# Kernel optimization log

Hardware: AMD Instinct MI355X
Metric: run time of the kernel (lower is better)

## Reference

```python
import jax, jax.numpy as jnp
import numpy as np

H = 8        # n_heads (== n_kv_heads)
D = 128      # head_dim
WINDOW = 16  # sliding window (left); causal => right window = 0
EPS = 1e-6   # qk_norm_eps


def rms_norm(x, w, eps=EPS):
    # RMSNorm over last dim with learnable scale
    ms = jnp.mean(jnp.square(x), axis=-1, keepdims=True)
    return x * jax.lax.rsqrt(ms + eps) * w


def setup_inputs() -> dict:
    key = jax.random.key(0)
    ks = jax.random.split(key, 5)
    B, S, dim = 4, 2048, 1024
    scale = 1.0 / np.sqrt(dim)
    return {
        "x": jax.random.normal(ks[0], (B, S, dim), jnp.float32),
        "wq": jax.random.normal(ks[1], (dim, dim), jnp.float32) * scale,
        "wk": jax.random.normal(ks[2], (dim, dim), jnp.float32) * scale,
        "wv": jax.random.normal(ks[3], (dim, dim), jnp.float32) * scale,
        "wo": jax.random.normal(ks[4], (dim, dim), jnp.float32) * scale,
        "q_norm_w": jnp.ones((dim,), jnp.float32),
        "k_norm_w": jnp.ones((dim,), jnp.float32),
    }


def reference(x, wq, wk, wv, wo, q_norm_w, k_norm_w):
    B, S, dim = x.shape
    # projections (torch Linear: x @ W.T)
    xq = rms_norm(x @ wq.T, q_norm_w)
    xk = rms_norm(x @ wk.T, k_norm_w)
    xv = x @ wv.T
    q = xq.reshape(B, S, H, D)
    k = xk.reshape(B, S, H, D)
    v = xv.reshape(B, S, H, D)

    # ALiBi slopes for 8 heads (power of two): 2^-1 .. 2^-8
    slopes = jnp.exp2(-jnp.arange(1, H + 1, dtype=jnp.float32))
    pos = jnp.arange(S)
    rel = pos[None, :] - pos[:, None]          # [S, S], rel[i, j] = j - i
    bias = slopes[:, None, None] * rel.astype(x.dtype)   # [H, S, S]
    masked = (rel > 0) | (rel < -WINDOW)       # causal + sliding window
    bias = jnp.where(masked[None], -jnp.inf, bias)

    scores = jnp.einsum('bqhd,bkhd->bhqk', q, k) / np.sqrt(D) + bias[None]
    attn = jax.nn.softmax(scores, axis=-1)
    out = jnp.einsum('bhqk,bkhd->bqhd', attn, v).reshape(B, S, H * D)
    return out @ wo.T
```

## Files before the change

kernel.cpp:

```cpp
#include <hip/hip_runtime.h>
#include <math.h>

#define NHEADS 8
#define HDIM   128
#define WIN    16
#define DIM    1024
#define QKVDIM 3072
#define SEQ    2048
#define BATCH  4
#define MROWS  (BATCH * SEQ)
#define RMS_EPS 1e-6f

typedef __bf16 bf16x8 __attribute__((ext_vector_type(8)));
typedef unsigned short u16x8 __attribute__((ext_vector_type(8)));
typedef float  f32x4  __attribute__((ext_vector_type(4)));

__device__ __forceinline__ unsigned short f2b(float f) {
    union { float f; unsigned u; } c; c.f = f;
    return (unsigned short)((c.u + 0x7FFFu + ((c.u >> 16) & 1u)) >> 16);
}
__device__ __forceinline__ float b2f(unsigned short u) {
    union { unsigned u; float f; } c; c.u = ((unsigned)u) << 16; return c.f;
}
__device__ __forceinline__ bf16x8 u2b(u16x8 u) {
    union { u16x8 u; bf16x8 b; } c; c.u = u; return c.b;
}

__device__ __forceinline__ void storec(unsigned short* p, float v) { *p = f2b(v); }
__device__ __forceinline__ void storec(float* p, float v) { *p = v; }

__global__ __launch_bounds__(256) void cast_all(const float* __restrict__ x,
                                                const float* __restrict__ w0,
                                                const float* __restrict__ w1,
                                                const float* __restrict__ w2,
                                                const float* __restrict__ w3,
                                                unsigned short* __restrict__ xb,
                                                unsigned short* __restrict__ wb,
                                                float* __restrict__ sumsq)
{
    const int b = blockIdx.x;
    const int t = threadIdx.x;
    if (b >= 12288) {
        ((float4*)sumsq)[(b - 12288) * 256 + t] = make_float4(0.f, 0.f, 0.f, 0.f);
        return;
    }
    const float* src;
    unsigned short* dst;
    int i;
    if (b < 8192) {
        i = b * 256 + t;
        src = x; dst = xb;
    } else {
        const int bb = b - 8192;
        const int which = bb >> 10;
        i = (bb & 1023) * 256 + t;
        src = which == 0 ? w0 : which == 1 ? w1 : which == 2 ? w2 : w3;
        dst = wb + (size_t)which * DIM * DIM;
    }
    const float4 v = ((const float4*)src)[i];
    ushort4 o;
    o.x = f2b(v.x); o.y = f2b(v.y); o.z = f2b(v.z); o.w = f2b(v.w);
    ((ushort4*)dst)[i] = o;
}

#define BARR do { asm volatile("s_barrier" ::: "memory"); __builtin_amdgcn_sched_barrier(0); } while (0)
#define WAITV(N) asm volatile("s_waitcnt vmcnt(" #N ")" ::: "memory")

#define LDA8(mh, b) { \
    _Pragma("unroll") for (int il = 0; il < 4; ++il) { \
        const int rr = (wm * 128 + (mh) * 64 + il * 16 + frow) * 64; \
        af[il][0] = *(const bf16x8*)&As[b][rr + cs0]; \
        af[il][1] = *(const bf16x8*)&As[b][rr + cs1]; \
    } }

#define LDB4(nh, b, bgr) { \
    _Pragma("unroll") for (int jl = 0; jl < 2; ++jl) { \
        const int rr = (wn * 64 + (nh) * 32 + jl * 16 + frow) * 64; \
        bgr[jl][0] = *(const bf16x8*)&Bs[b][rr + cs0]; \
        bgr[jl][1] = *(const bf16x8*)&Bs[b][rr + cs1]; \
    } }

#define MMA16(mh, nh, bgr) { \
    __builtin_amdgcn_s_setprio(1); \
    _Pragma("unroll") for (int il = 0; il < 4; ++il) \
    _Pragma("unroll") for (int jl = 0; jl < 2; ++jl) { \
        acc[(mh)*4+il][(nh)*2+jl] = __builtin_amdgcn_mfma_f32_16x16x32_bf16(af[il][0], bgr[jl][0], acc[(mh)*4+il][(nh)*2+jl], 0, 0, 0); \
        acc[(mh)*4+il][(nh)*2+jl] = __builtin_amdgcn_mfma_f32_16x16x32_bf16(af[il][1], bgr[jl][1], acc[(mh)*4+il][(nh)*2+jl], 0, 0, 0); \
    } \
    __builtin_amdgcn_s_setprio(0); }

#define STAGE_A(b, half, kt) { \
    _Pragma("unroll") for (int s2 = 0; s2 < 2; ++s2) { \
        const int rb = (half) * 128 + s2 * 64; \
        __builtin_amdgcn_global_load_lds( \
            (const __attribute__((address_space(1))) void*)(gA + (size_t)rb * K + (kt)), \
            (__attribute__((address_space(3))) void*)&As[b][(rb + wid * 8) * 64], 16, 0, 0); \
    } }

#define STAGE_B(b, half, kt) { \
    _Pragma("unroll") for (int s2 = 0; s2 < 2; ++s2) { \
        const int rb = (half) * 128 + s2 * 64; \
        __builtin_amdgcn_global_load_lds( \
            (const __attribute__((address_space(1))) void*)(gB + (size_t)rb * K + (kt)), \
            (__attribute__((address_space(3))) void*)&Bs[b][(rb + wid * 8) * 64], 16, 0, 0); \
    } }

template <typename TC>
__global__ __launch_bounds__(512, 2) void gemm_nt_256(const unsigned short* __restrict__ A,
                                                      const unsigned short* __restrict__ B,
                                                      TC* __restrict__ C,
                                                      float* __restrict__ sumsq,
                                                      int M, int N, int K)
{
    __shared__ __align__(16) __bf16 As[2][256 * 64];
    __shared__ __align__(16) __bf16 Bs[2][256 * 64];

    const int t    = threadIdx.x;
    const int wid  = t >> 6;
    const int lane = t & 63;
    const int wm   = wid >> 2;
    const int wn   = wid & 3;
    const int bm0  = blockIdx.y * 256;
    const int bn0  = blockIdx.x * 256;

    const int frow = lane & 15;
    const int quad = lane >> 4;
    const int cs0  = ((quad    ) ^ (frow & 7)) * 8;
    const int cs1  = ((quad + 4) ^ (frow & 7)) * 8;

    const int lr = lane >> 3;
    const int lc = (lane & 7) ^ lr;
    const unsigned short* gA = A + (size_t)(bm0 + wid * 8 + lr) * K + lc * 8;
    const unsigned short* gB = B + (size_t)(bn0 + wid * 8 + lr) * K + lc * 8;

    f32x4 acc[8][4];
    #pragma unroll
    for (int i = 0; i < 8; ++i)
        #pragma unroll
        for (int j = 0; j < 4; ++j)
            #pragma unroll
            for (int e = 0; e < 4; ++e) acc[i][j][e] = 0.f;

    bf16x8 af[4][2], bg0[2][2], bg1[2][2];

    const int NI = K >> 7;

    STAGE_B(0, 0, 0); STAGE_B(0, 1, 0); STAGE_A(0, 0, 0); STAGE_A(0, 1, 0);
    STAGE_B(1, 0, 64); STAGE_B(1, 1, 64);
    WAITV(4);
    BARR;

    for (int i = 0; i < NI; ++i) {
        const bool last = (i == NI - 1);
        const int kt0 = i << 7;
        LDA8(0, 0); LDB4(0, 0, bg0);
        STAGE_A(1, 0, kt0 + 64);
        BARR; MMA16(0, 0, bg0); BARR;
        LDB4(1, 0, bg1);
        STAGE_A(1, 1, kt0 + 64);
        BARR; MMA16(0, 1, bg1); BARR;
        LDA8(1, 0);
        if (!last) STAGE_B(0, 0, kt0 + 128);
        BARR; MMA16(1, 1, bg1); BARR;
        if (!last) STAGE_B(0, 1, kt0 + 128);
        BARR; MMA16(1, 0, bg0);
        if (last) { WAITV(0); } else { WAITV(4); }
        BARR;
        LDA8(0, 1); LDB4(0, 1, bg0);
        if (!last) STAGE_A(0, 0, kt0 + 128);
        BARR; MMA16(0, 0, bg0); BARR;
        LDB4(1, 1, bg1);
        if (!last) STAGE_A(0, 1, kt0 + 128);
        BARR; MMA16(0, 1, bg1); BARR;
        LDA8(1, 1);
        if (!last) STAGE_B(1, 0, kt0 + 192);
        BARR; MMA16(1, 1, bg1); BARR;
        if (!last) STAGE_B(1, 1, kt0 + 192);
        BARR; MMA16(1, 0, bg0);
        if (!last) { WAITV(4); }
        BARR;
    }

    const int m_base = bm0 + wm * 128;
    const int n_base = bn0 + wn * 64;
    #pragma unroll
    for (int i2 = 0; i2 < 8; ++i2)
        #pragma unroll
        for (int r = 0; r < 4; ++r) {
            TC* crow = C + (size_t)(m_base + i2 * 16 + quad * 4 + r) * N + n_base + frow;
            #pragma unroll
            for (int j = 0; j < 4; ++j)
                storec(crow + j * 16, acc[i2][j][r]);
        }

    if (sumsq != nullptr && bn0 < 2 * DIM) {
        const int which = bn0 >> 10;
        #pragma unroll
        for (int i2 = 0; i2 < 8; ++i2)
            #pragma unroll
            for (int r = 0; r < 4; ++r) {
                float p = acc[i2][0][r] * acc[i2][0][r] + acc[i2][1][r] * acc[i2][1][r]
                        + acc[i2][2][r] * acc[i2][2][r] + acc[i2][3][r] * acc[i2][3][r];
                p += __shfl_xor(p, 1, 64);
                p += __shfl_xor(p, 2, 64);
                p += __shfl_xor(p, 4, 64);
                p += __shfl_xor(p, 8, 64);
                if (frow == 0)
                    atomicAdd(&sumsq[(size_t)(m_base + i2 * 16 + quad * 4 + r) * 2 + which], p);
            }
    }
}

__global__ __launch_bounds__(256) void attn_mfma(const unsigned short* __restrict__ qkv,
                                                 const float* __restrict__ sumsq,
                                                 const float* __restrict__ qw,
                                                 const float* __restrict__ kw,
                                                 unsigned short* __restrict__ o)
{
    __shared__ __align__(16) unsigned short Klds[80 * 136];
    __shared__ __align__(16) unsigned short Vt[128 * 88];
    __shared__ __align__(16) unsigned short Plds[4 * 16 * 40];

    const int t  = threadIdx.x;
    const int qb = blockIdx.x;
    const int h  = blockIdx.y;
    const int r0 = qb * 64;
    const int i0 = r0 & (SEQ - 1);
    const int bb = r0 - i0;

    const unsigned short* kg = qkv + DIM + h * HDIM;
    const unsigned short* vg = qkv + 2 * DIM + h * HDIM;

    #pragma unroll
    for (int it = 0; it < 5; ++it) {
        const int c = it * 256 + t;
        {
            const int lr2 = c >> 4, c8 = c & 15;
            const int ks = i0 - 16 + lr2;
            const int rc = ks < 0 ? 0 : ks;
            const float ksc = rsqrtf(sumsq[(size_t)(bb + rc) * 2 + 1] * (1.0f / DIM) + RMS_EPS);
            const u16x8 kv = *(const u16x8*)(kg + (size_t)(bb + rc) * QKVDIM + c8 * 8);
            u16x8 ko;
            #pragma unroll
            for (int e = 0; e < 8; ++e)
                ko[e] = f2b(b2f(kv[e]) * ksc * kw[h * HDIM + c8 * 8 + e]);
            *(u16x8*)&Klds[lr2 * 136 + c8 * 8] = ko;
        }
        {
            const int c8 = c / 80, lr2 = c - c8 * 80;
            const int ks = i0 - 16 + lr2;
            const int rc = ks < 0 ? 0 : ks;
            const u16x8 vv = *(const u16x8*)(vg + (size_t)(bb + rc) * QKVDIM + c8 * 8);
            #pragma unroll
            for (int e = 0; e < 8; ++e)
                Vt[(c8 * 8 + e) * 88 + lr2] = vv[e];
        }
    }
    __syncthreads();

    const int w    = t >> 6;
    const int lane = t & 63;
    const int frow = lane & 15;
    const int quad = lane >> 4;
    const int fk   = quad * 8;

    f32x4 s0 = {0.f, 0.f, 0.f, 0.f}, s1 = {0.f, 0.f, 0.f, 0.f};
    const unsigned short* qg = qkv + h * HDIM;
    const size_t qrow = (size_t)(r0 + w * 16 + frow) * QKVDIM;
    const float qsc = rsqrtf(sumsq[(size_t)(r0 + w * 16 + frow) * 2] * (1.0f / DIM) + RMS_EPS);
    #pragma unroll
    for (int kt = 0; kt < 4; ++kt) {
        const u16x8 qa = *(const u16x8*)(qg + qrow + kt * 32 + fk);
        u16x8 qn;
        #pragma unroll
        for (int e = 0; e < 8; ++e)
            qn[e] = f2b(b2f(qa[e]) * qsc * qw[h * HDIM + kt * 32 + fk + e]);
        const bf16x8 af = u2b(qn);
        const bf16x8 b0 = *(const bf16x8*)&Klds[(w * 16 + frow) * 136 + kt * 32 + fk];
        const bf16x8 b1 = *(const bf16x8*)&Klds[(w * 16 + 16 + frow) * 136 + kt * 32 + fk];
        s0 = __builtin_amdgcn_mfma_f32_16x16x32_bf16(af, b0, s0, 0, 0, 0);
        s1 = __builtin_amdgcn_mfma_f32_16x16x32_bf16(af, b1, s1, 0, 0, 0);
    }

    const float scl   = 0.088388347648318447f;
    const float slope = exp2f(-(float)(h + 1));
    const bool  lead  = (i0 == 0) && (w == 0);
    const int   col   = frow;
    float inv[4];
    #pragma unroll
    for (int r = 0; r < 4; ++r) {
        const int m = quad * 4 + r;
        float v0 = (col < m || lead) ? -1e30f : s0[r] * scl + slope * (float)(col - 16 - m);
        float v1 = (col > m)         ? -1e30f : s1[r] * scl + slope * (float)(col - m);
        float mx = fmaxf(v0, v1);
        #pragma unroll
        for (int off = 1; off < 16; off <<= 1) mx = fmaxf(mx, __shfl_xor(mx, off, 64));
        const float e0 = __expf(v0 - mx);
        const float e1 = __expf(v1 - mx);
        float sm = e0 + e1;
        #pragma unroll
        for (int off = 1; off < 16; off <<= 1) sm += __shfl_xor(sm, off, 64);
        inv[r] = 1.0f / sm;
        Plds[(w * 16 + m) * 40 + col]      = f2b(e0);
        Plds[(w * 16 + m) * 40 + 16 + col] = f2b(e1);
    }

    const bf16x8 pf = *(const bf16x8*)&Plds[(w * 16 + frow) * 40 + fk];
    f32x4 oa[8];
    #pragma unroll
    for (int nt = 0; nt < 8; ++nt) {
        oa[nt][0] = 0.f; oa[nt][1] = 0.f; oa[nt][2] = 0.f; oa[nt][3] = 0.f;
        const bf16x8 vf = *(const bf16x8*)&Vt[(nt * 16 + frow) * 88 + w * 16 + fk];
        oa[nt] = __builtin_amdgcn_mfma_f32_16x16x32_bf16(pf, vf, oa[nt], 0, 0, 0);
    }

    #pragma unroll
    for (int nt = 0; nt < 8; ++nt)
        #pragma unroll
        for (int r = 0; r < 4; ++r) {
            const int m = quad * 4 + r;
            o[(size_t)(r0 + w * 16 + m) * DIM + h * HDIM + nt * 16 + col] =
                f2b(oa[nt][r] * inv[r]);
        }
}

extern "C" void kernel_launch(void* const* d_in, const int* in_sizes, int n_in,
                              void* d_out, int out_size, void* d_ws, size_t ws_size,
                              hipStream_t stream)
{
    const float* x  = (const float*)d_in[0];
    const float* wq = (const float*)d_in[1];
    const float* wk = (const float*)d_in[2];
    const float* wv = (const float*)d_in[3];
    const float* wo = (const float*)d_in[4];
    const float* qw = (const float*)d_in[5];
    const float* kw = (const float*)d_in[6];
    float* out = (float*)d_out;

    unsigned short* xb   = (unsigned short*)d_ws;
    unsigned short* wb   = xb + (size_t)MROWS * DIM;
    unsigned short* xqkv = wb + (size_t)4 * DIM * DIM;
    unsigned short* ob   = xqkv + (size_t)MROWS * QKVDIM;
    float*          ssq  = (float*)(ob + (size_t)MROWS * DIM);
    unsigned short* wob  = wb + (size_t)3 * DIM * DIM;

    cast_all<<<12304, 256, 0, stream>>>(x, wq, wk, wv, wo, xb, wb, ssq);

    gemm_nt_256<unsigned short><<<dim3(QKVDIM / 256, MROWS / 256), 512, 0, stream>>>(
        xb, wb, xqkv, ssq, MROWS, QKVDIM, DIM);

    attn_mfma<<<dim3(MROWS / 64, NHEADS), 256, 0, stream>>>(xqkv, ssq, qw, kw, ob);

    gemm_nt_256<float><<<dim3(DIM / 256, MROWS / 256), 512, 0, stream>>>(
        ob, wob, out, nullptr, MROWS, DIM, DIM);
}
```

Baseline: 227.3 us.

## Fold QK RMS-norm scales into scores and use 128-tile GEMM for output projection

```diff
diff --git a/kernel.cpp b/kernel.cpp
--- a/kernel.cpp
+++ b/kernel.cpp
@@ -211,13 +211,113 @@
     }
 }
 
+template <typename TC>
+__global__ __launch_bounds__(256) void gemm_nt_mfma(const unsigned short* __restrict__ A,
+                                                    const unsigned short* __restrict__ B,
+                                                    TC* __restrict__ C,
+                                                    float* __restrict__ sumsq,
+                                                    int M, int N, int K)
+{
+    __shared__ __align__(16) __bf16 As[128 * 64];
+    __shared__ __align__(16) __bf16 Bs[128 * 64];
+
+    const int t    = threadIdx.x;
+    const int w    = t >> 6;
+    const int lane = t & 63;
+    const int wm   = w >> 1;
+    const int wn   = w & 1;
+    const int bm0  = blockIdx.y * 128;
+    const int bn0  = blockIdx.x * 128;
+
+    const int lrow   = lane >> 3;
+    const int lchunk = (lane & 7) ^ (lrow & 7);
+    const size_t laneoff = (size_t)lrow * K + lchunk * 8;
+
+    const unsigned short* gA = A + (size_t)bm0 * K + laneoff;
+    const unsigned short* gB = B + (size_t)bn0 * K + laneoff;
+
+    const int frow = lane & 15;
+    const int quad = lane >> 4;
+    const int cs0 = ((quad    ) ^ (frow & 7)) * 8;
+    const int cs1 = ((quad + 4) ^ (frow & 7)) * 8;
+
+    f32x4 acc[4][4];
+    #pragma unroll
+    for (int i = 0; i < 4; ++i)
+        #pragma unroll
+        for (int j = 0; j < 4; ++j)
+            #pragma unroll
+            for (int e = 0; e < 4; ++e) acc[i][j][e] = 0.f;
+
+    for (int kt = 0; kt < K; kt += 64) {
+        __syncthreads();
+        #pragma unroll
+        for (int s = 0; s < 4; ++s) {
+            const int seg = w * 4 + s;
+            __builtin_amdgcn_global_load_lds(
+                (const __attribute__((address_space(1))) void*)(gA + (size_t)seg * 8 * K + kt),
+                (__attribute__((address_space(3))) void*)&As[seg * 512], 16, 0, 0);
+            __builtin_amdgcn_global_load_lds(
+                (const __attribute__((address_space(1))) void*)(gB + (size_t)seg * 8 * K + kt),
+                (__attribute__((address_space(3))) void*)&Bs[seg * 512], 16, 0, 0);
+        }
+        __syncthreads();
+
+        #pragma unroll
+        for (int sub = 0; sub < 2; ++sub) {
+            const int cs = sub ? cs1 : cs0;
+            bf16x8 af[4], bg[4];
+            #pragma unroll
+            for (int i = 0; i < 4; ++i) {
+                af[i] = *(const bf16x8*)&As[(wm * 64 + i * 16 + frow) * 64 + cs];
+                bg[i] = *(const bf16x8*)&Bs[(wn * 64 + i * 16 + frow) * 64 + cs];
+            }
+            #pragma unroll
+            for (int i = 0; i < 4; ++i)
+                #pragma unroll
+                for (int j = 0; j < 4; ++j)
+                    acc[i][j] = __builtin_amdgcn_mfma_f32_16x16x32_bf16(af[i], bg[j], acc[i][j], 0, 0, 0);
+        }
+    }
+
+    const int m_base = bm0 + wm * 64;
+    const int n_base = bn0 + wn * 64;
+    const int col    = frow;
+    const int rquad  = quad * 4;
+    #pragma unroll
+    for (int i = 0; i < 4; ++i)
+        #pragma unroll
+        for (int r = 0; r < 4; ++r) {
+            TC* crow = C + (size_t)(m_base + i * 16 + rquad + r) * N + n_base + col;
+            #pragma unroll
+            for (int j = 0; j < 4; ++j)
+                storec(crow + j * 16, acc[i][j][r]);
+        }
+
+    if (sumsq != nullptr && bn0 < 2 * DIM) {
+        const int which = bn0 >> 10;
+        #pragma unroll
+        for (int i = 0; i < 4; ++i)
+            #pragma unroll
+            for (int r = 0; r < 4; ++r) {
+                float p = acc[i][0][r] * acc[i][0][r] + acc[i][1][r] * acc[i][1][r]
+                        + acc[i][2][r] * acc[i][2][r] + acc[i][3][r] * acc[i][3][r];
+                p += __shfl_xor(p, 1, 64);
+                p += __shfl_xor(p, 2, 64);
+                p += __shfl_xor(p, 4, 64);
+                p += __shfl_xor(p, 8, 64);
+                if (frow == 0)
+                    atomicAdd(&sumsq[(size_t)(m_base + i * 16 + rquad + r) * 2 + which], p);
+            }
+    }
+}
+
 __global__ __launch_bounds__(256) void attn_mfma(const unsigned short* __restrict__ qkv,
                                                  const float* __restrict__ sumsq,
                                                  const float* __restrict__ qw,
                                                  const float* __restrict__ kw,
                                                  unsigned short* __restrict__ o)
 {
-    __shared__ __align__(16) unsigned short Klds[80 * 136];
     __shared__ __align__(16) unsigned short Vt[128 * 88];
     __shared__ __align__(16) unsigned short Plds[4 * 16 * 40];
 
@@ -228,35 +328,19 @@
     const int i0 = r0 & (SEQ - 1);
     const int bb = r0 - i0;
 
-    const unsigned short* kg = qkv + DIM + h * HDIM;
     const unsigned short* vg = qkv + 2 * DIM + h * HDIM;
 
     #pragma unroll
     for (int it = 0; it < 5; ++it) {
         const int c = it * 256 + t;
-        {
-            const int lr2 = c >> 4, c8 = c & 15;
-            const int ks = i0 - 16 + lr2;
-            const int rc = ks < 0 ? 0 : ks;
-            const float ksc = rsqrtf(sumsq[(size_t)(bb + rc) * 2 + 1] * (1.0f / DIM) + RMS_EPS);
-            const u16x8 kv = *(const u16x8*)(kg + (size_t)(bb + rc) * QKVDIM + c8 * 8);
-            u16x8 ko;
-            #pragma unroll
-            for (int e = 0; e < 8; ++e)
-                ko[e] = f2b(b2f(kv[e]) * ksc * kw[h * HDIM + c8 * 8 + e]);
-            *(u16x8*)&Klds[lr2 * 136 + c8 * 8] = ko;
-        }
-        {
-            const int c8 = c / 80, lr2 = c - c8 * 80;
-            const int ks = i0 - 16 + lr2;
-            const int rc = ks < 0 ? 0 : ks;
-            const u16x8 vv = *(const u16x8*)(vg + (size_t)(bb + rc) * QKVDIM + c8 * 8);
-            #pragma unroll
-            for (int e = 0; e < 8; ++e)
-                Vt[(c8 * 8 + e) * 88 + lr2] = vv[e];
-        }
-    }
-    __syncthreads();
+        const int c8 = c / 80, lr2 = c - c8 * 80;
+        const int ks = i0 - 16 + lr2;
+        const int rc = ks < 0 ? 0 : ks;
+        const u16x8 vv = *(const u16x8*)(vg + (size_t)(bb + rc) * QKVDIM + c8 * 8);
+        #pragma unroll
+        for (int e = 0; e < 8; ++e)
+            Vt[(c8 * 8 + e) * 88 + lr2] = vv[e];
+    }
 
     const int w    = t >> 6;
     const int lane = t & 63;
@@ -264,23 +348,37 @@
     const int quad = lane >> 4;
     const int fk   = quad * 8;
 
+    const unsigned short* qg = qkv + h * HDIM;
+    const unsigned short* kg = qkv + DIM + h * HDIM;
+    const size_t qrow = (size_t)(r0 + w * 16 + frow) * QKVDIM;
+    const int kidx0   = i0 - 16 + w * 16 + frow;
+    const int kr0     = kidx0 < 0 ? 0 : kidx0;
+    const size_t krow0 = (size_t)(bb + kr0) * QKVDIM;
+    const size_t krow1 = (size_t)(r0 + w * 16 + frow) * QKVDIM;
+
     f32x4 s0 = {0.f, 0.f, 0.f, 0.f}, s1 = {0.f, 0.f, 0.f, 0.f};
-    const unsigned short* qg = qkv + h * HDIM;
-    const size_t qrow = (size_t)(r0 + w * 16 + frow) * QKVDIM;
-    const float qsc = rsqrtf(sumsq[(size_t)(r0 + w * 16 + frow) * 2] * (1.0f / DIM) + RMS_EPS);
     #pragma unroll
     for (int kt = 0; kt < 4; ++kt) {
         const u16x8 qa = *(const u16x8*)(qg + qrow + kt * 32 + fk);
         u16x8 qn;
         #pragma unroll
-        for (int e = 0; e < 8; ++e)
-            qn[e] = f2b(b2f(qa[e]) * qsc * qw[h * HDIM + kt * 32 + fk + e]);
+        for (int e = 0; e < 8; ++e) {
+            const int d = h * HDIM + kt * 32 + fk + e;
+            qn[e] = f2b(b2f(qa[e]) * qw[d] * kw[d]);
+        }
         const bf16x8 af = u2b(qn);
-        const bf16x8 b0 = *(const bf16x8*)&Klds[(w * 16 + frow) * 136 + kt * 32 + fk];
-        const bf16x8 b1 = *(const bf16x8*)&Klds[(w * 16 + 16 + frow) * 136 + kt * 32 + fk];
+        const bf16x8 b0 = *(const bf16x8*)(kg + krow0 + kt * 32 + fk);
+        const bf16x8 b1 = *(const bf16x8*)(kg + krow1 + kt * 32 + fk);
         s0 = __builtin_amdgcn_mfma_f32_16x16x32_bf16(af, b0, s0, 0, 0, 0);
         s1 = __builtin_amdgcn_mfma_f32_16x16x32_bf16(af, b1, s1, 0, 0, 0);
     }
+
+    const float ksc0 = rsqrtf(sumsq[(size_t)(bb + kr0) * 2 + 1] * (1.0f / DIM) + RMS_EPS);
+    const float ksc1 = rsqrtf(sumsq[(size_t)(r0 + w * 16 + frow) * 2 + 1] * (1.0f / DIM) + RMS_EPS);
+    float qs[4];
+    #pragma unroll
+    for (int r = 0; r < 4; ++r)
+        qs[r] = rsqrtf(sumsq[(size_t)(r0 + w * 16 + quad * 4 + r) * 2] * (1.0f / DIM) + RMS_EPS);
 
     const float scl   = 0.088388347648318447f;
     const float slope = exp2f(-(float)(h + 1));
@@ -290,8 +388,10 @@
     #pragma unroll
     for (int r = 0; r < 4; ++r) {
         const int m = quad * 4 + r;
-        float v0 = (col < m || lead) ? -1e30f : s0[r] * scl + slope * (float)(col - 16 - m);
-        float v1 = (col > m)         ? -1e30f : s1[r] * scl + slope * (float)(col - m);
+        const float sc0 = scl * qs[r] * ksc0;
+        const float sc1 = scl * qs[r] * ksc1;
+        float v0 = (col < m || lead) ? -1e30f : s0[r] * sc0 + slope * (float)(col - 16 - m);
+        float v1 = (col > m)         ? -1e30f : s1[r] * sc1 + slope * (float)(col - m);
         float mx = fmaxf(v0, v1);
         #pragma unroll
         for (int off = 1; off < 16; off <<= 1) mx = fmaxf(mx, __shfl_xor(mx, off, 64));
@@ -304,6 +404,8 @@
         Plds[(w * 16 + m) * 40 + col]      = f2b(e0);
         Plds[(w * 16 + m) * 40 + 16 + col] = f2b(e1);
     }
+
+    __syncthreads();
 
     const bf16x8 pf = *(const bf16x8*)&Plds[(w * 16 + frow) * 40 + fk];
     f32x4 oa[8];
@@ -351,6 +453,6 @@
 
     attn_mfma<<<dim3(MROWS / 64, NHEADS), 256, 0, stream>>>(xqkv, ssq, qw, kw, ob);
 
-    gemm_nt_256<float><<<dim3(DIM / 256, MROWS / 256), 512, 0, stream>>>(
+    gemm_nt_mfma<float><<<dim3(DIM / 128, MROWS / 128), 256, 0, stream>>>(
         ob, wob, out, nullptr, MROWS, DIM, DIM);
 }
```

Result: faster. 220.3 us (-3.0%).
